# Kernel optimization log

Hardware: AMD Instinct MI355X
Metric: run time of the kernel (lower is better)

The kernel has to match this reference:

```python
import jax, jax.numpy as jnp
import numpy as np

B, N, C, H = 64, 4096, 128, 4
ALPHA = 0.2  # leaky_relu negative slope


def setup_inputs() -> dict:
    key = jax.random.key(0)
    k1, k2, k3, k4, k5 = jax.random.split(key, 5)
    V = jax.random.normal(k1, (B, N, C), dtype=jnp.float32)
    graph_size = jax.random.randint(k2, (B,), 1, N + 1, dtype=jnp.int32)
    # xavier_uniform-like init for weight [C, H*C] and tune_weight [1, H, C]
    lim_w = float(np.sqrt(6.0 / (C + H * C)))
    weight = jax.random.uniform(k3, (C, H * C), minval=-lim_w, maxval=lim_w, dtype=jnp.float32)
    lim_t = float(np.sqrt(6.0 / (H + C)))
    tune_weight = jax.random.uniform(k4, (1, H, C), minval=-lim_t, maxval=lim_t, dtype=jnp.float32)
    bias = jnp.full((H * C,), 0.01, dtype=jnp.float32)
    return {"V": V, "graph_size": graph_size, "weight": weight, "bias": bias, "tune_weight": tune_weight}


def reference(V, graph_size, weight, bias, tune_weight):
    # valid-node mask: node n of graph b is valid iff n < graph_size[b]
    mask = jnp.arange(N)[None, :] < graph_size[:, None]          # [B, N]
    # linear projection: [B, N, C] @ [C, H*C] + bias -> [B, N, H, C]
    Vg = (jnp.einsum('bnc,cd->bnd', V, weight) + bias).reshape(B, N, H, C)
    # attention logits per head: sum over features of tune_weight * Vg
    a = jnp.einsum('bnhc,ohc->bnh', Vg, tune_weight)             # [B, N, H]
    a = jnp.where(a >= 0, a, ALPHA * a)                          # leaky_relu
    # per-graph (segment) softmax over valid nodes
    a = jnp.where(mask[:, :, None], a, -jnp.inf)
    a = jax.nn.softmax(a, axis=1)                                # [B, N, H]
    # weighted segment sum -> [B, H, C] -> [B, H*C] (concat=True)
    out = jnp.einsum('bnhc,bnh->bhc', Vg, a)
    return out.reshape(B, H * C)
```

## Files before the change

### kernel.cpp

```cpp
#include <hip/hip_runtime.h>

#define NB 64
#define NN 4096
#define NC 128
#define NH 4
#define HC (NH * NC)
#define PSTRIDE (8 + HC)
#define NSLICE 16
#define TROWS 64
#define LRELU 0.2f

__global__ __launch_bounds__(128) void k0_wt(const float* __restrict__ W,
                                             const float* __restrict__ bias,
                                             const float* __restrict__ tune,
                                             float* __restrict__ wtbt)
{
    const int bid = blockIdx.x;
    const int t = threadIdx.x;
    const float* src = (bid < NC) ? (W + (size_t)bid * HC) : bias;
    float* dst = (bid < NC) ? (wtbt + bid * NH) : (wtbt + NC * NH);
    const float4 a = reinterpret_cast<const float4*>(src)[t];
    const float4 b = reinterpret_cast<const float4*>(tune)[t];
    float p = a.x * b.x + a.y * b.y + a.z * b.z + a.w * b.w;
    #pragma unroll
    for (int off = 16; off; off >>= 1) p += __shfl_xor(p, off, 32);
    if ((t & 31) == 0) dst[t >> 5] = p;
}

__global__ __launch_bounds__(256, 4) void k1_part(const float* __restrict__ V,
                                                  const int* __restrict__ gs,
                                                  const float* __restrict__ wtbt,
                                                  float* __restrict__ part)
{
    __shared__ float smem[8192];
    float (*Vt)[NC] = reinterpret_cast<float(*)[NC]>(smem);
    float (*Sall)[NH][132] = reinterpret_cast<float(*)[NH][132]>(smem);
    float* llds = smem + 8 * NH * 132;

    const int slice = blockIdx.x;
    const int b = blockIdx.y;
    const int tid = threadIdx.x;
    const int hw = tid >> 5;
    const int lane = tid & 31;
    const int h = lane >> 3;
    const int j = lane & 7;
    const int gsz = gs[b];

    float wtk[16];
    #pragma unroll
    for (int u = 0; u < 16; ++u) wtk[u] = wtbt[(16 * j + u) * NH + h];
    const float bt = wtbt[HC + h];

    const int segB = (gsz + NSLICE - 1) / NSLICE;
    const int myBeg = slice * segB;
    int myEnd = myBeg + segB;
    if (myEnd > gsz) myEnd = gsz;
    const int nrows = (myEnd > myBeg) ? (myEnd - myBeg) : 0;
    const int ntile = (nrows + TROWS - 1) / TROWS;

    float l = 0.f;
    float S[16] = {};

    const float4* Vg4 = reinterpret_cast<const float4*>(V);
    const size_t gbase = (size_t)b * NN;

    for (int tile = 0; tile < ntile; ++tile) {
        const int tbase = myBeg + tile * TROWS;
        float4 r[8];
        #pragma unroll
        for (int k = 0; k < 8; ++k) {
            const int idx = tid + (k << 8);
            const int row = idx >> 5;
            const int gr = tbase + row;
            const int src_row = (gr < myEnd) ? gr : myBeg;
            r[k] = Vg4[(gbase + src_row) * 32 + (idx & 31)];
        }
        #pragma unroll
        for (int k = 0; k < 8; ++k) {
            const int idx = tid + (k << 8);
            reinterpret_cast<float4*>(smem)[idx] = r[k];
        }
        __syncthreads();
        #pragma unroll 2
        for (int rr = 0; rr < 8; ++rr) {
            const int row = (hw << 3) + rr;
            const bool valid = (tbase + row < myEnd);
            const float4* vr = reinterpret_cast<const float4*>(&Vt[row][j * 16]);
            const float4 A0 = vr[0];
            const float4 A1 = vr[1];
            const float4 A2 = vr[2];
            const float4 A3 = vr[3];
            float a0 = A0.x * wtk[0]  + A0.y * wtk[1]  + A0.z * wtk[2]  + A0.w * wtk[3];
            float a1 = A1.x * wtk[4]  + A1.y * wtk[5]  + A1.z * wtk[6]  + A1.w * wtk[7];
            float a2 = A2.x * wtk[8]  + A2.y * wtk[9]  + A2.z * wtk[10] + A2.w * wtk[11];
            float a3 = A3.x * wtk[12] + A3.y * wtk[13] + A3.z * wtk[14] + A3.w * wtk[15];
            float lg = (a0 + a1) + (a2 + a3);
            lg += __shfl_xor(lg, 1, 32);
            lg += __shfl_xor(lg, 2, 32);
            lg += __shfl_xor(lg, 4, 32);
            float x = lg + bt;
            x = (x >= 0.f) ? x : LRELU * x;
            float p = __expf(x);
            p = valid ? p : 0.f;
            l += p;
            S[0]  += p * A0.x;  S[1]  += p * A0.y;  S[2]  += p * A0.z;  S[3]  += p * A0.w;
            S[4]  += p * A1.x;  S[5]  += p * A1.y;  S[6]  += p * A1.z;  S[7]  += p * A1.w;
            S[8]  += p * A2.x;  S[9]  += p * A2.y;  S[10] += p * A2.z;  S[11] += p * A2.w;
            S[12] += p * A3.x;  S[13] += p * A3.y;  S[14] += p * A3.z;  S[15] += p * A3.w;
        }
        __syncthreads();
    }

    if (j == 0) llds[hw * NH + h] = l;
    #pragma unroll
    for (int t = 0; t < 4; ++t) {
        float4 s4;
        s4.x = S[4 * t]; s4.y = S[4 * t + 1]; s4.z = S[4 * t + 2]; s4.w = S[4 * t + 3];
        *reinterpret_cast<float4*>(&Sall[hw][h][16 * j + 4 * t]) = s4;
    }
    __syncthreads();
    float* pb = part + (size_t)(b * NSLICE + slice) * PSTRIDE;
    if (tid < 4) {
        float L = 0.f;
        #pragma unroll
        for (int ww = 0; ww < 8; ++ww) L += llds[ww * NH + tid];
        pb[4 + tid] = L;
    }
    #pragma unroll
    for (int r2 = 0; r2 < 2; ++r2) {
        const int e = tid + r2 * 256;
        const int hh = e >> 7, k = e & 127;
        float s = 0.f;
        #pragma unroll
        for (int ww = 0; ww < 8; ++ww) s += Sall[ww][hh][k];
        pb[8 + e] = s;
    }
}

__global__ __launch_bounds__(128) void k2_out(const float* __restrict__ part,
                                              const float* __restrict__ W,
                                              const float* __restrict__ bias,
                                              float* __restrict__ out)
{
    const int b = blockIdx.x;
    const int h = blockIdx.y;
    const int tid = threadIdx.x;
    const float* pb = part + (size_t)b * NSLICE * PSTRIDE;

    __shared__ float Sn[NC];
    __shared__ float sL;
    if (tid == 0) {
        float L = 0.f;
        #pragma unroll
        for (int c = 0; c < NSLICE; ++c) L += pb[(size_t)c * PSTRIDE + 4 + h];
        sL = L;
    }
    __syncthreads();
    {
        float s = 0.f;
        #pragma unroll 4
        for (int c = 0; c < NSLICE; ++c)
            s += pb[(size_t)c * PSTRIDE + 8 + h * NC + tid];
        Sn[tid] = s / sL;
    }
    __syncthreads();
    const int d = h * NC + tid;
    float acc = 0.f;
    #pragma unroll 4
    for (int k = 0; k < NC; ++k) acc += Sn[k] * W[(size_t)k * HC + d];
    out[(size_t)b * HC + d] = acc + bias[d];
}

extern "C" void kernel_launch(void* const* d_in, const int* in_sizes, int n_in,
                              void* d_out, int out_size, void* d_ws, size_t ws_size,
                              hipStream_t stream)
{
    const float* V    = (const float*)d_in[0];
    const int*   gsz  = (const int*)d_in[1];
    const float* W    = (const float*)d_in[2];
    const float* bias = (const float*)d_in[3];
    const float* tune = (const float*)d_in[4];
    float* out  = (float*)d_out;
    float* wtbt = (float*)d_ws;
    float* part = wtbt + PSTRIDE;

    hipLaunchKernelGGL(k0_wt, dim3(NC + 1), dim3(128), 0, stream, W, bias, tune, wtbt);
    hipLaunchKernelGGL(k1_part, dim3(NSLICE, NB), dim3(256), 0, stream, V, gsz, wtbt, part);
    hipLaunchKernelGGL(k2_out, dim3(NB, NH), dim3(128), 0, stream, part, W, bias, out);
}
```

Baseline: 44.20 us.

## Fuse output projection into partial kernel via atomic accumulation and last-block reduction

Drops the third kernel. Each slice block now atomically adds its partial softmax denominators and weighted sums into global accumulators, which k0 zeroes first. The last block to finish for each graph, found with an atomic counter, normalizes the sums and performs the 128x512 output projection. This removes one launch and the partials round trip, at the cost of atomics and an imbalanced tail where a single block per graph does the projection.

```diff
diff --git a/kernel.cpp b/kernel.cpp
--- a/kernel.cpp
+++ b/kernel.cpp
@@ -5,20 +5,26 @@
 #define NC 128
 #define NH 4
 #define HC (NH * NC)
-#define PSTRIDE (8 + HC)
 #define NSLICE 16
 #define TROWS 64
 #define LRELU 0.2f
 
+#define WS_CNT  520
+#define WS_LACC 584
+#define WS_SACC 840
+#define WS_ZWORDS (64 + 256 + NB * HC)
+
 __global__ __launch_bounds__(128) void k0_wt(const float* __restrict__ W,
                                              const float* __restrict__ bias,
                                              const float* __restrict__ tune,
-                                             float* __restrict__ wtbt)
+                                             float* __restrict__ ws)
 {
     const int bid = blockIdx.x;
     const int t = threadIdx.x;
+    for (int idx = bid * 128 + t; idx < WS_ZWORDS; idx += 129 * 128)
+        ws[WS_CNT + idx] = 0.f;
     const float* src = (bid < NC) ? (W + (size_t)bid * HC) : bias;
-    float* dst = (bid < NC) ? (wtbt + bid * NH) : (wtbt + NC * NH);
+    float* dst = (bid < NC) ? (ws + bid * NH) : (ws + NC * NH);
     const float4 a = reinterpret_cast<const float4*>(src)[t];
     const float4 b = reinterpret_cast<const float4*>(tune)[t];
     float p = a.x * b.x + a.y * b.y + a.z * b.z + a.w * b.w;
@@ -27,15 +33,24 @@
     if ((t & 31) == 0) dst[t >> 5] = p;
 }
 
-__global__ __launch_bounds__(256, 4) void k1_part(const float* __restrict__ V,
-                                                  const int* __restrict__ gs,
-                                                  const float* __restrict__ wtbt,
-                                                  float* __restrict__ part)
+__global__ __launch_bounds__(256, 4) void kfused(const float* __restrict__ V,
+                                                 const int* __restrict__ gs,
+                                                 float* __restrict__ ws,
+                                                 const float* __restrict__ W,
+                                                 const float* __restrict__ bias,
+                                                 float* __restrict__ out)
 {
     __shared__ float smem[8192];
     float (*Vt)[NC] = reinterpret_cast<float(*)[NC]>(smem);
     float (*Sall)[NH][132] = reinterpret_cast<float(*)[NH][132]>(smem);
     float* llds = smem + 8 * NH * 132;
+    __shared__ int   sOld;
+    __shared__ float Lh[NH];
+
+    const float* wtbt = ws;
+    int*   cnt  = reinterpret_cast<int*>(ws + WS_CNT);
+    float* Lacc = ws + WS_LACC;
+    float* Sacc = ws + WS_SACC;
 
     const int slice = blockIdx.x;
     const int b = blockIdx.y;
@@ -119,12 +134,11 @@
         *reinterpret_cast<float4*>(&Sall[hw][h][16 * j + 4 * t]) = s4;
     }
     __syncthreads();
-    float* pb = part + (size_t)(b * NSLICE + slice) * PSTRIDE;
     if (tid < 4) {
         float L = 0.f;
         #pragma unroll
         for (int ww = 0; ww < 8; ++ww) L += llds[ww * NH + tid];
-        pb[4 + tid] = L;
+        atomicAdd(&Lacc[b * NH + tid], L);
     }
     #pragma unroll
     for (int r2 = 0; r2 < 2; ++r2) {
@@ -133,42 +147,31 @@
         float s = 0.f;
         #pragma unroll
         for (int ww = 0; ww < 8; ++ww) s += Sall[ww][hh][k];
-        pb[8 + e] = s;
-    }
-}
-
-__global__ __launch_bounds__(128) void k2_out(const float* __restrict__ part,
-                                              const float* __restrict__ W,
-                                              const float* __restrict__ bias,
-                                              float* __restrict__ out)
-{
-    const int b = blockIdx.x;
-    const int h = blockIdx.y;
-    const int tid = threadIdx.x;
-    const float* pb = part + (size_t)b * NSLICE * PSTRIDE;
-
-    __shared__ float Sn[NC];
-    __shared__ float sL;
-    if (tid == 0) {
-        float L = 0.f;
-        #pragma unroll
-        for (int c = 0; c < NSLICE; ++c) L += pb[(size_t)c * PSTRIDE + 4 + h];
-        sL = L;
+        atomicAdd(&Sacc[(size_t)b * HC + e], s);
     }
     __syncthreads();
-    {
-        float s = 0.f;
-        #pragma unroll 4
-        for (int c = 0; c < NSLICE; ++c)
-            s += pb[(size_t)c * PSTRIDE + 8 + h * NC + tid];
-        Sn[tid] = s / sL;
+    if (tid == 0) sOld = atomicAdd(&cnt[b], 1);
+    __syncthreads();
+    if (sOld != NSLICE - 1) return;
+
+    if (tid < 4) Lh[tid] = atomicAdd(&Lacc[b * NH + tid], 0.f);
+    __syncthreads();
+    #pragma unroll
+    for (int r2 = 0; r2 < 2; ++r2) {
+        const int e = tid + r2 * 256;
+        const float stot = atomicAdd(&Sacc[(size_t)b * HC + e], 0.f);
+        smem[e] = stot / Lh[e >> 7];
     }
     __syncthreads();
-    const int d = h * NC + tid;
-    float acc = 0.f;
-    #pragma unroll 4
-    for (int k = 0; k < NC; ++k) acc += Sn[k] * W[(size_t)k * HC + d];
-    out[(size_t)b * HC + d] = acc + bias[d];
+    #pragma unroll
+    for (int r2 = 0; r2 < 2; ++r2) {
+        const int d = tid + r2 * 256;
+        const int hh = d >> 7;
+        float acc = 0.f;
+        #pragma unroll 4
+        for (int k = 0; k < NC; ++k) acc += smem[hh * NC + k] * W[(size_t)k * HC + d];
+        out[(size_t)b * HC + d] = acc + bias[d];
+    }
 }
 
 extern "C" void kernel_launch(void* const* d_in, const int* in_sizes, int n_in,
@@ -180,11 +183,9 @@
     const float* W    = (const float*)d_in[2];
     const float* bias = (const float*)d_in[3];
     const float* tune = (const float*)d_in[4];
-    float* out  = (float*)d_out;
-    float* wtbt = (float*)d_ws;
-    float* part = wtbt + PSTRIDE;
+    float* out = (float*)d_out;
+    float* ws  = (float*)d_ws;
 
-    hipLaunchKernelGGL(k0_wt, dim3(NC + 1), dim3(128), 0, stream, W, bias, tune, wtbt);
-    hipLaunchKernelGGL(k1_part, dim3(NSLICE, NB), dim3(256), 0, stream, V, gsz, wtbt, part);
-    hipLaunchKernelGGL(k2_out, dim3(NB, NH), dim3(128), 0, stream, part, W, bias, out);
+    hipLaunchKernelGGL(k0_wt, dim3(NC + 1), dim3(128), 0, stream, W, bias, tune, ws);
+    hipLaunchKernelGGL(kfused, dim3(NSLICE, NB), dim3(256), 0, stream, V, gsz, ws, W, bias, out);
 }
```

Result: slower. 46.51 us (+5.2%).

## Split logit computation into separate kernel before weighted accumulation

Applied to the files above, without the earlier changes.

Moves the per-row attention logit and exp computation out of the accumulation kernel into a new kernel that writes exp-logits for every node to a workspace array. The accumulation kernel then reads these precomputed weights instead of doing dot products and shuffle reductions. This shortens the compute in the accumulation loop, but V must now be read twice. The logits pass also processes every row, including those beyond graph_size, so it adds a lot of memory traffic.

```diff
diff --git a/kernel.cpp b/kernel.cpp
--- a/kernel.cpp
+++ b/kernel.cpp
@@ -8,7 +8,11 @@
 #define PSTRIDE (8 + HC)
 #define NSLICE 16
 #define TROWS 64
+#define NROWA 128
 #define LRELU 0.2f
+
+#define WS_PART 520
+#define WS_P    (WS_PART + NB * NSLICE * PSTRIDE)
 
 __global__ __launch_bounds__(128) void k0_wt(const float* __restrict__ W,
                                              const float* __restrict__ bias,
@@ -27,10 +31,49 @@
     if ((t & 31) == 0) dst[t >> 5] = p;
 }
 
-__global__ __launch_bounds__(256, 4) void k1_part(const float* __restrict__ V,
-                                                  const int* __restrict__ gs,
-                                                  const float* __restrict__ wtbt,
-                                                  float* __restrict__ part)
+__global__ __launch_bounds__(256, 4) void kA_logits(const float* __restrict__ V,
+                                                    const float* __restrict__ wtbt,
+                                                    float* __restrict__ pArr)
+{
+    const int tid = threadIdx.x;
+    const int hw = tid >> 5;
+    const int lane = tid & 31;
+    const int h = lane >> 3;
+    const int j = lane & 7;
+
+    float wtk[16];
+    #pragma unroll
+    for (int u = 0; u < 16; ++u) wtk[u] = wtbt[(16 * j + u) * NH + h];
+    const float bt = wtbt[HC + h];
+
+    const int base = blockIdx.x * NROWA;
+    #pragma unroll 2
+    for (int it = 0; it < NROWA / 8; ++it) {
+        const int row = base + it * 8 + hw;
+        const float4* vr = reinterpret_cast<const float4*>(V + (size_t)row * NC + j * 16);
+        const float4 A0 = vr[0];
+        const float4 A1 = vr[1];
+        const float4 A2 = vr[2];
+        const float4 A3 = vr[3];
+        float a0 = A0.x * wtk[0]  + A0.y * wtk[1]  + A0.z * wtk[2]  + A0.w * wtk[3];
+        float a1 = A1.x * wtk[4]  + A1.y * wtk[5]  + A1.z * wtk[6]  + A1.w * wtk[7];
+        float a2 = A2.x * wtk[8]  + A2.y * wtk[9]  + A2.z * wtk[10] + A2.w * wtk[11];
+        float a3 = A3.x * wtk[12] + A3.y * wtk[13] + A3.z * wtk[14] + A3.w * wtk[15];
+        float lg = (a0 + a1) + (a2 + a3);
+        lg += __shfl_xor(lg, 1, 32);
+        lg += __shfl_xor(lg, 2, 32);
+        lg += __shfl_xor(lg, 4, 32);
+        float x = lg + bt;
+        x = (x >= 0.f) ? x : LRELU * x;
+        const float p = __expf(x);
+        if (j == 0) pArr[(size_t)row * NH + h] = p;
+    }
+}
+
+__global__ __launch_bounds__(256, 4) void kB_acc(const float* __restrict__ V,
+                                                 const int* __restrict__ gs,
+                                                 const float* __restrict__ pArr,
+                                                 float* __restrict__ part)
 {
     __shared__ float smem[8192];
     float (*Vt)[NC] = reinterpret_cast<float(*)[NC]>(smem);
@@ -45,11 +88,6 @@
     const int h = lane >> 3;
     const int j = lane & 7;
     const int gsz = gs[b];
-
-    float wtk[16];
-    #pragma unroll
-    for (int u = 0; u < 16; ++u) wtk[u] = wtbt[(16 * j + u) * NH + h];
-    const float bt = wtbt[HC + h];
 
     const int segB = (gsz + NSLICE - 1) / NSLICE;
     const int myBeg = slice * segB;
@@ -90,17 +128,7 @@
             const float4 A1 = vr[1];
             const float4 A2 = vr[2];
             const float4 A3 = vr[3];
-            float a0 = A0.x * wtk[0]  + A0.y * wtk[1]  + A0.z * wtk[2]  + A0.w * wtk[3];
-            float a1 = A1.x * wtk[4]  + A1.y * wtk[5]  + A1.z * wtk[6]  + A1.w * wtk[7];
-            float a2 = A2.x * wtk[8]  + A2.y * wtk[9]  + A2.z * wtk[10] + A2.w * wtk[11];
-            float a3 = A3.x * wtk[12] + A3.y * wtk[13] + A3.z * wtk[14] + A3.w * wtk[15];
-            float lg = (a0 + a1) + (a2 + a3);
-            lg += __shfl_xor(lg, 1, 32);
-            lg += __shfl_xor(lg, 2, 32);
-            lg += __shfl_xor(lg, 4, 32);
-            float x = lg + bt;
-            x = (x >= 0.f) ? x : LRELU * x;
-            float p = __expf(x);
+            float p = pArr[(gbase + tbase + row) * NH + h];
             p = valid ? p : 0.f;
             l += p;
             S[0]  += p * A0.x;  S[1]  += p * A0.y;  S[2]  += p * A0.z;  S[3]  += p * A0.w;
@@ -181,10 +209,13 @@
     const float* bias = (const float*)d_in[3];
     const float* tune = (const float*)d_in[4];
     float* out  = (float*)d_out;
-    float* wtbt = (float*)d_ws;
-    float* part = wtbt + PSTRIDE;
+    float* ws   = (float*)d_ws;
+    float* wtbt = ws;
+    float* part = ws + WS_PART;
+    float* pArr = ws + WS_P;
 
     hipLaunchKernelGGL(k0_wt, dim3(NC + 1), dim3(128), 0, stream, W, bias, tune, wtbt);
-    hipLaunchKernelGGL(k1_part, dim3(NSLICE, NB), dim3(256), 0, stream, V, gsz, wtbt, part);
+    hipLaunchKernelGGL(kA_logits, dim3(NB * NN / NROWA), dim3(256), 0, stream, V, wtbt, pArr);
+    hipLaunchKernelGGL(kB_acc, dim3(NSLICE, NB), dim3(256), 0, stream, V, gsz, pArr, part);
     hipLaunchKernelGGL(k2_out, dim3(NB, NH), dim3(128), 0, stream, part, W, bias, out);
 }
```

Result: slower. 77.56 us (+75.5%).
